# Kernel tuning notes

Hardware: AMD Instinct MI355X
Metric: run time of the kernel (lower is better)

The kernel has to match this reference:

```python
import jax, jax.numpy as jnp
import numpy as np

EMBED = 1024
HEADS = 16
HEAD_DIM = EMBED // HEADS


def setup_inputs() -> dict:
    key = jax.random.key(0)
    k1, k2, k3, k4, k5 = jax.random.split(key, 5)
    B, S = 4, 2048
    scale = 1.0 / np.sqrt(EMBED)
    return {
        "query_features": jax.random.normal(k1, (B, S, EMBED), dtype=jnp.float32),
        "W_qkv": jax.random.normal(k2, (EMBED, 3 * EMBED), dtype=jnp.float32) * scale,
        "b_qkv": jnp.zeros((3 * EMBED,), dtype=jnp.float32),
        "W_out": jax.random.normal(k3, (EMBED, EMBED), dtype=jnp.float32) * scale,
        "b_out": jnp.zeros((EMBED,), dtype=jnp.float32),
    }


def reference(query_features, W_qkv, b_qkv, W_out, b_out):
    B, S, E = query_features.shape
    qkv = jnp.einsum("bse,ef->bsf", query_features, W_qkv) + b_qkv  # [B,S,3E]
    q, k, v = jnp.split(qkv, 3, axis=-1)
    # split heads: [B,H,S,D]
    def heads(x):
        return x.reshape(B, S, HEADS, HEAD_DIM).transpose(0, 2, 1, 3)
    q, k, v = heads(q), heads(k), heads(v)
    scale = 1.0 / np.sqrt(HEAD_DIM)
    scores = jnp.einsum("bhqd,bhkd->bhqk", q, k) * scale
    attn = jax.nn.softmax(scores, axis=-1)
    out = jnp.einsum("bhqk,bhkd->bhqd", attn, v)  # [B,H,S,D]
    out = out.transpose(0, 2, 1, 3).reshape(B, S, E)
    return jnp.einsum("bse,ef->bsf", out, W_out) + b_out
```

## Files before the change

### kernel.cpp

```cpp
#include <hip/hip_runtime.h>
#include <hip/hip_bf16.h>
#include <stdint.h>
#include <stddef.h>

using short8  = __attribute__((ext_vector_type(8))) short;
using short4v = __attribute__((ext_vector_type(4))) short;
using int4v   = __attribute__((ext_vector_type(4))) int;
using f32x4   = __attribute__((ext_vector_type(4))) float;
typedef __hip_bfloat16 bf16_t;

__device__ __forceinline__ void glds16(const void* g, const void* l) {
  __builtin_amdgcn_global_load_lds(
      (const __attribute__((address_space(1))) void*)g,
      (__attribute__((address_space(3))) void*)l, 16, 0, 0);
}
__device__ __forceinline__ short bfbits(float x) {
  bf16_t h = __float2bfloat16(x);
  return __builtin_bit_cast(short, h);
}
__device__ __forceinline__ int pk2(float lo, float hi) {
  return __builtin_amdgcn_perm(__builtin_bit_cast(unsigned, hi),
                               __builtin_bit_cast(unsigned, lo), 0x07060302u);
}

__global__ __launch_bounds__(256)
void preprocess(const void* __restrict__ Wqkv, bf16_t* __restrict__ WqkvT,
                const void* __restrict__ Wout, bf16_t* __restrict__ WoutT,
                const void* __restrict__ Xv, bf16_t* __restrict__ Xb,
                int* __restrict__ flag) {
  __shared__ int sbad;
  __shared__ float tile[32][33];
  const int tid = threadIdx.x;
  const int bid = blockIdx.x;
  if (tid == 0) sbad = 0;
  __syncthreads();
  {
    int bad = 0;
    const unsigned short* wp = (const unsigned short*)Wqkv;
#pragma unroll
    for (int j = 0; j < 4; ++j) {
      float f = __uint_as_float((unsigned)wp[tid + j * 256] << 16);
      if (!(fabsf(f) <= 1e10f)) bad = 1;
    }
    if (bad) sbad = 1;
  }
  __syncthreads();
  const int isf = sbad;
  if (bid == 0 && tid == 0) *flag = isf;

  if (bid < 4096) {
    int bx = bid & 127;
    const int by = bid >> 7;
    const int tx = tid & 31, ty = tid >> 5;
    const void* Wv;
    bf16_t* Wt;
    int C;
    if (bx < 96) {
      Wv = Wqkv; Wt = WqkvT; C = 3072;
    } else {
      bx -= 96; Wv = Wout; Wt = WoutT; C = 1024;
    }
    const int n0 = bx * 32, k0 = by * 32;
#pragma unroll
    for (int j = 0; j < 4; ++j) {
      const int k = k0 + ty + j * 8;
      tile[ty + j * 8][tx] =
          isf ? ((const float*)Wv)[(size_t)k * C + n0 + tx]
              : __bfloat162float(((const bf16_t*)Wv)[(size_t)k * C + n0 + tx]);
    }
    __syncthreads();
#pragma unroll
    for (int j = 0; j < 4; ++j) {
      const int n = n0 + ty + j * 8;
      Wt[(size_t)n * 1024 + k0 + tx] = __float2bfloat16(tile[tx][ty + j * 8]);
    }
  } else {
    const int i = ((bid - 4096) * 256 + tid) * 4;
    if (isf) {
      const float4 v = *(const float4*)((const float*)Xv + i);
      Xb[i + 0] = __float2bfloat16(v.x);
      Xb[i + 1] = __float2bfloat16(v.y);
      Xb[i + 2] = __float2bfloat16(v.z);
      Xb[i + 3] = __float2bfloat16(v.w);
    } else {
      *(uint2*)(Xb + i) = *(const uint2*)((const bf16_t*)Xv + i);
    }
  }
}

template <int MODE>
__global__ __launch_bounds__(256)
void gemm_k(const bf16_t* __restrict__ A, const bf16_t* __restrict__ Bt,
            const void* __restrict__ biasv, void* __restrict__ Cv,
            bf16_t* __restrict__ Qo, bf16_t* __restrict__ Ko,
            bf16_t* __restrict__ Vo, int M, int N, int K,
            const int* __restrict__ flag) {
  constexpr float CSC = 0.18033688011112042f;
  __shared__ __align__(16) bf16_t lA[2][128 * 64];
  __shared__ __align__(16) bf16_t lB[2][128 * 64];

  const int isf32 = *flag;
  const int tid  = threadIdx.x;
  const int w    = tid >> 6;
  const int lane = tid & 63;
  const int lrow = lane & 15;
  const int quad = lane >> 4;
  const int m0 = blockIdx.x * 128;
  const int n0 = blockIdx.y * 128;
  const int wm = (w >> 1) * 64;
  const int wn = (w & 1) * 64;

  f32x4 acc[4][4];
  for (int i = 0; i < 4; ++i)
    for (int j = 0; j < 4; ++j)
      for (int r = 0; r < 4; ++r) acc[i][j][r] = 0.f;

  const char* Ab = (const char*)A;
  const char* Bb = (const char*)Bt;
  unsigned aoff[4], boff[4];
  int ldst[4];
#pragma unroll
  for (int i = 0; i < 4; ++i) {
    const int cbase = i * 256 + w * 64;
    const int c = cbase + lane;
    const int row = c >> 3;
    const int q = (c & 7) ^ (row & 7);
    aoff[i] = (unsigned)((m0 + row) * K + q * 8) * 2u;
    boff[i] = (unsigned)((n0 + row) * K + q * 8) * 2u;
    ldst[i] = cbase * 16;
  }

  auto stage = [&](int buf, int kt) {
    const unsigned kb = (unsigned)kt * 2u;
#pragma unroll
    for (int i = 0; i < 4; ++i) {
      glds16(Ab + aoff[i] + kb, (const char*)lA[buf] + ldst[i]);
      glds16(Bb + boff[i] + kb, (const char*)lB[buf] + ldst[i]);
    }
  };

  stage(0, 0);
  __syncthreads();

  int buf = 0;
  for (int kt = 0; kt < K; kt += 64) {
    if (kt + 64 < K) stage(buf ^ 1, kt + 64);
    const char* la = (const char*)lA[buf];
    const char* lb = (const char*)lB[buf];
#pragma unroll
    for (int ks = 0; ks < 2; ++ks) {
      short8 af[4], bfr[4];
#pragma unroll
      for (int mi = 0; mi < 4; ++mi) {
        const int row = wm + mi * 16 + lrow;
        const int slot = (ks * 4 + quad) ^ (row & 7);
        af[mi] = *(const short8*)(la + row * 128 + slot * 16);
      }
#pragma unroll
      for (int ni = 0; ni < 4; ++ni) {
        const int row = wn + ni * 16 + lrow;
        const int slot = (ks * 4 + quad) ^ (row & 7);
        bfr[ni] = *(const short8*)(lb + row * 128 + slot * 16);
      }
#pragma unroll
      for (int mi = 0; mi < 4; ++mi)
#pragma unroll
        for (int ni = 0; ni < 4; ++ni)
          acc[mi][ni] = __builtin_amdgcn_mfma_f32_16x16x32_bf16(
              af[mi], bfr[ni], acc[mi][ni], 0, 0, 0);
    }
    __syncthreads();
    buf ^= 1;
  }

  if (MODE == 1) {
    const int sec = n0 >> 10;
    const int b = m0 >> 11;
    const int s0 = (m0 & 2047) + wm + quad * 4;
#pragma unroll
    for (int mi = 0; mi < 4; ++mi) {
#pragma unroll
      for (int ni = 0; ni < 4; ++ni) {
        const int col = n0 + wn + ni * 16 + lrow;
        const float bv = isf32 ? ((const float*)biasv)[col]
                               : __bfloat162float(((const bf16_t*)biasv)[col]);
        const int h = (col >> 6) & 15, d = col & 63;
        const int s = s0 + mi * 16;
        if (sec == 2) {
          short4v hv4;
#pragma unroll
          for (int r = 0; r < 4; ++r) hv4[r] = bfbits(acc[mi][ni][r] + bv);
          *(short4v*)(Vo + ((((size_t)b * 16 + h) * 64) + d) * 2048 + s) = hv4;
        } else if (sec == 0) {
          bf16_t* dst = Qo + ((((size_t)b * 16 + h) * 2048) + s) * 64 + d;
#pragma unroll
          for (int r = 0; r < 4; ++r)
            dst[(size_t)r * 64] = __float2bfloat16((acc[mi][ni][r] + bv) * CSC);
        } else {
          bf16_t* dst = Ko + ((((size_t)b * 16 + h) * 2048) + s) * 64 + d;
#pragma unroll
          for (int r = 0; r < 4; ++r)
            dst[(size_t)r * 64] = __float2bfloat16(acc[mi][ni][r] + bv);
        }
      }
    }
  } else {
#pragma unroll
    for (int mi = 0; mi < 4; ++mi) {
#pragma unroll
      for (int ni = 0; ni < 4; ++ni) {
        const int col = n0 + wn + ni * 16 + lrow;
        const float bv = isf32 ? ((const float*)biasv)[col]
                               : __bfloat162float(((const bf16_t*)biasv)[col]);
#pragma unroll
        for (int r = 0; r < 4; ++r) {
          const int row = m0 + wm + mi * 16 + quad * 4 + r;
          const float val = acc[mi][ni][r] + bv;
          if (isf32)
            ((float*)Cv)[(size_t)row * N + col] = val;
          else
            ((bf16_t*)Cv)[(size_t)row * N + col] = __float2bfloat16(val);
        }
      }
    }
  }
}

__global__ __launch_bounds__(256, 2)
void attn_fwd(const bf16_t* __restrict__ Q, const bf16_t* __restrict__ K,
              const bf16_t* __restrict__ Vt, bf16_t* __restrict__ AO) {
  __shared__ __align__(16) bf16_t lK[2][64 * 64];
  __shared__ __align__(16) bf16_t lV[2][64 * 64];

  const int tid  = threadIdx.x;
  const int w    = tid >> 6;
  const int lane = tid & 63;
  const int lrow = lane & 15;
  const int quad = lane >> 4;
  const int id = blockIdx.x;
  const int swz = (id & 7) * 64 + (id >> 3);
  const int bh  = swz >> 3;
  const int q0  = (swz & 7) * 256;

  const bf16_t* Qb = Q + (size_t)bh * 2048 * 64;
  const bf16_t* Kb = K + (size_t)bh * 2048 * 64;
  const bf16_t* Vb = Vt + (size_t)bh * 64 * 2048;

  const int rbase = (lrow >> 2) * 8 + (lrow & 3);
  const int fkl   = 2 * (lrow >> 2) + (lrow & 1);

  short8 aq[4][2];
#pragma unroll
  for (int qt = 0; qt < 4; ++qt)
#pragma unroll
    for (int ks = 0; ks < 2; ++ks)
      aq[qt][ks] = *(const short8*)(Qb +
          (size_t)(q0 + w * 64 + qt * 16 + lrow) * 64 + ks * 32 + quad * 8);

  short8 ones;
#pragma unroll
  for (int j = 0; j < 8; ++j) ones[j] = (short)0x3F80;

  const f32x4 zf = {0.f, 0.f, 0.f, 0.f};

  f32x4 ot[4][4];
  f32x4 lsacc[4];
#pragma unroll
  for (int dt = 0; dt < 4; ++dt)
#pragma unroll
    for (int qt = 0; qt < 4; ++qt)
#pragma unroll
      for (int r = 0; r < 4; ++r) ot[dt][qt][r] = 0.f;
#pragma unroll
  for (int qt = 0; qt < 4; ++qt)
#pragma unroll
    for (int r = 0; r < 4; ++r) lsacc[qt][r] = 0.f;

  auto stage = [&](int buf, int kt) {
#pragma unroll
    for (int i = 0; i < 2; ++i) {
      const int cbase = i * 256 + w * 64;
      const int c = cbase + lane;
      const int row = c >> 3, ch = c & 7;
      const int fk = 2 * ((row >> 3) & 3) + (row & 1);
      glds16(Kb + (size_t)(kt + row) * 64 + (ch ^ fk) * 8,
             (const char*)lK[buf] + cbase * 16);
      glds16(Vb + (size_t)row * 2048 + kt + (ch ^ (row & 7)) * 8,
             (const char*)lV[buf] + cbase * 16);
    }
  };

  auto compute = [&](const bf16_t* lKb, const bf16_t* lVb) {
    f32x4 sc[2][2][4];
#pragma unroll
    for (int g = 0; g < 2; ++g) {
      short8 ak0[2], ak1[2];
#pragma unroll
      for (int T = 0; T < 2; ++T) {
        const int row = g * 32 + T * 4 + rbase;
        ak0[T] = *(const short8*)((const char*)lKb + row * 128 +
                                  ((0 * 4 + quad) ^ fkl) * 16);
        ak1[T] = *(const short8*)((const char*)lKb + row * 128 +
                                  ((1 * 4 + quad) ^ fkl) * 16);
      }
      __builtin_amdgcn_s_setprio(1);
#pragma unroll
      for (int T = 0; T < 2; ++T)
#pragma unroll
        for (int qt = 0; qt < 4; ++qt)
          sc[g][T][qt] = __builtin_amdgcn_mfma_f32_16x16x32_bf16(
              ak0[T], aq[qt][0], zf, 0, 0, 0);
#pragma unroll
      for (int T = 0; T < 2; ++T)
#pragma unroll
        for (int qt = 0; qt < 4; ++qt)
          sc[g][T][qt] = __builtin_amdgcn_mfma_f32_16x16x32_bf16(
              ak1[T], aq[qt][1], sc[g][T][qt], 0, 0, 0);
      __builtin_amdgcn_s_setprio(0);
    }
#pragma unroll
    for (int g = 0; g < 2; ++g) {
      short8 pb[4];
#pragma unroll
      for (int qt = 0; qt < 4; ++qt) {
        float p[8];
#pragma unroll
        for (int T = 0; T < 2; ++T)
#pragma unroll
          for (int r = 0; r < 4; ++r)
            p[T * 4 + r] = __builtin_amdgcn_exp2f(sc[g][T][qt][r]);
        int4v pi = {pk2(p[0], p[1]), pk2(p[2], p[3]), pk2(p[4], p[5]),
                    pk2(p[6], p[7])};
        pb[qt] = __builtin_bit_cast(short8, pi);
      }

      __builtin_amdgcn_s_setprio(1);
#pragma unroll
      for (int qt = 0; qt < 4; ++qt)
        lsacc[qt] = __builtin_amdgcn_mfma_f32_16x16x32_bf16(ones, pb[qt],
                                                            lsacc[qt], 0, 0, 0);
#pragma unroll
      for (int dt = 0; dt < 4; ++dt) {
        const int row = dt * 16 + lrow;
        const int slot = (g * 4 + quad) ^ (row & 7);
        const short8 vf =
            *(const short8*)((const char*)lVb + row * 128 + slot * 16);
#pragma unroll
        for (int qt = 0; qt < 4; ++qt)
          ot[dt][qt] = __builtin_amdgcn_mfma_f32_16x16x32_bf16(
              vf, pb[qt], ot[dt][qt], 0, 0, 0);
      }
      __builtin_amdgcn_s_setprio(0);
    }
  };

  stage(0, 0);
  __syncthreads();

  for (int kt = 0; kt < 2048; kt += 128) {
    if (kt + 64 < 2048) stage(1, kt + 64);
    compute(lK[0], lV[0]);
    __syncthreads();
    if (kt + 128 < 2048) stage(0, kt + 128);
    compute(lK[1], lV[1]);
    __syncthreads();
  }

  const int b = bh >> 4, h = bh & 15;
#pragma unroll
  for (int qt = 0; qt < 4; ++qt) {
    const float inv = 1.f / lsacc[qt][0];
    const int srow = q0 + w * 64 + qt * 16 + lrow;
#pragma unroll
    for (int dt = 0; dt < 4; ++dt) {
      uint2 pack;
      short* ps = (short*)&pack;
#pragma unroll
      for (int r = 0; r < 4; ++r) ps[r] = bfbits(ot[dt][qt][r] * inv);
      *(uint2*)(AO + ((size_t)b * 2048 + srow) * 1024 + h * 64 + dt * 16 +
                quad * 4) = pack;
    }
  }
}

extern "C" void kernel_launch(void* const* d_in, const int* in_sizes, int n_in,
                              void* d_out, int out_size, void* d_ws,
                              size_t ws_size, hipStream_t stream) {
  const void* X    = d_in[0];
  const void* Wqkv = d_in[1];
  const void* bqkv = d_in[2];
  const void* Wout = d_in[3];
  const void* bout = d_in[4];

  char* ws = (char*)d_ws;
  bf16_t* WqkvT = (bf16_t*)(ws);
  bf16_t* WoutT = (bf16_t*)(ws + 6291456);
  bf16_t* Qw    = (bf16_t*)(ws + 8388608);
  bf16_t* Kw    = (bf16_t*)(ws + 25165824);
  bf16_t* Vw    = (bf16_t*)(ws + 41943040);
  bf16_t* AOw   = (bf16_t*)(ws + 58720256);
  bf16_t* Xbf   = AOw;
  int*    flag  = (int*)(ws + 75497472);

  preprocess<<<12288, 256, 0, stream>>>(Wqkv, WqkvT, Wout, WoutT, X, Xbf, flag);

  gemm_k<1><<<dim3(64, 24), 256, 0, stream>>>(Xbf, WqkvT, bqkv, nullptr, Qw,
                                              Kw, Vw, 8192, 3072, 1024, flag);
  attn_fwd<<<512, 256, 0, stream>>>(Qw, Kw, Vw, AOw);
  gemm_k<0><<<dim3(64, 8), 256, 0, stream>>>(AOw, WoutT, bout, d_out, nullptr,
                                             nullptr, nullptr, 8192, 1024, 1024,
                                             flag);
}
```

Before: 258.1 us.

## Enlarge GEMM block tile to 256x128 with 512 threads, single-buffered LDS

The GEMM kernel now uses 8 waves per block covering a 256x128 output tile instead of 4 waves covering 128x128, so each B tile loaded into LDS is reused across more rows and the grid has half as many blocks. The LDS double buffer is dropped: each k-step loads into a single buffer, synchronizes, computes, then synchronizes again. This cuts LDS footprint and global reloads of B, but loads no longer overlap with MFMA work. The output-projection GEMM grid becomes only 256 blocks, which may underfill the device.

```diff
diff --git a/kernel.cpp b/kernel.cpp
--- a/kernel.cpp
+++ b/kernel.cpp
@@ -89,15 +89,15 @@
 }
 
 template <int MODE>
-__global__ __launch_bounds__(256)
+__global__ __launch_bounds__(512)
 void gemm_k(const bf16_t* __restrict__ A, const bf16_t* __restrict__ Bt,
             const void* __restrict__ biasv, void* __restrict__ Cv,
             bf16_t* __restrict__ Qo, bf16_t* __restrict__ Ko,
             bf16_t* __restrict__ Vo, int M, int N, int K,
             const int* __restrict__ flag) {
   constexpr float CSC = 0.18033688011112042f;
-  __shared__ __align__(16) bf16_t lA[2][128 * 64];
-  __shared__ __align__(16) bf16_t lB[2][128 * 64];
+  __shared__ __align__(16) bf16_t lA[256 * 64];
+  __shared__ __align__(16) bf16_t lB[128 * 64];
 
   const int isf32 = *flag;
   const int tid  = threadIdx.x;
@@ -105,7 +105,7 @@
   const int lane = tid & 63;
   const int lrow = lane & 15;
   const int quad = lane >> 4;
-  const int m0 = blockIdx.x * 128;
+  const int m0 = blockIdx.x * 256;
   const int n0 = blockIdx.y * 128;
   const int wm = (w >> 1) * 64;
   const int wn = (w & 1) * 64;
@@ -117,36 +117,38 @@
 
   const char* Ab = (const char*)A;
   const char* Bb = (const char*)Bt;
-  unsigned aoff[4], boff[4];
-  int ldst[4];
+  unsigned aoff[4], boff[2];
+  int lda[4], ldb[2];
 #pragma unroll
   for (int i = 0; i < 4; ++i) {
-    const int cbase = i * 256 + w * 64;
-    const int c = cbase + lane;
+    const int c = i * 512 + tid;
     const int row = c >> 3;
     const int q = (c & 7) ^ (row & 7);
     aoff[i] = (unsigned)((m0 + row) * K + q * 8) * 2u;
+    lda[i] = c * 16;
+  }
+#pragma unroll
+  for (int i = 0; i < 2; ++i) {
+    const int c = i * 512 + tid;
+    const int row = c >> 3;
+    const int q = (c & 7) ^ (row & 7);
     boff[i] = (unsigned)((n0 + row) * K + q * 8) * 2u;
-    ldst[i] = cbase * 16;
-  }
-
-  auto stage = [&](int buf, int kt) {
+    ldb[i] = c * 16;
+  }
+
+  auto stage = [&](int kt) {
     const unsigned kb = (unsigned)kt * 2u;
 #pragma unroll
-    for (int i = 0; i < 4; ++i) {
-      glds16(Ab + aoff[i] + kb, (const char*)lA[buf] + ldst[i]);
-      glds16(Bb + boff[i] + kb, (const char*)lB[buf] + ldst[i]);
-    }
+    for (int i = 0; i < 4; ++i)
+      glds16(Ab + aoff[i] + kb, (const char*)lA + lda[i]);
+#pragma unroll
+    for (int i = 0; i < 2; ++i)
+      glds16(Bb + boff[i] + kb, (const char*)lB + ldb[i]);
   };
 
-  stage(0, 0);
-  __syncthreads();
-
-  int buf = 0;
   for (int kt = 0; kt < K; kt += 64) {
-    if (kt + 64 < K) stage(buf ^ 1, kt + 64);
-    const char* la = (const char*)lA[buf];
-    const char* lb = (const char*)lB[buf];
+    stage(kt);
+    __syncthreads();
 #pragma unroll
     for (int ks = 0; ks < 2; ++ks) {
       short8 af[4], bfr[4];
@@ -154,13 +156,13 @@
       for (int mi = 0; mi < 4; ++mi) {
         const int row = wm + mi * 16 + lrow;
         const int slot = (ks * 4 + quad) ^ (row & 7);
-        af[mi] = *(const short8*)(la + row * 128 + slot * 16);
+        af[mi] = *(const short8*)((const char*)lA + row * 128 + slot * 16);
       }
 #pragma unroll
       for (int ni = 0; ni < 4; ++ni) {
         const int row = wn + ni * 16 + lrow;
         const int slot = (ks * 4 + quad) ^ (row & 7);
-        bfr[ni] = *(const short8*)(lb + row * 128 + slot * 16);
+        bfr[ni] = *(const short8*)((const char*)lB + row * 128 + slot * 16);
       }
 #pragma unroll
       for (int mi = 0; mi < 4; ++mi)
@@ -170,7 +172,6 @@
               af[mi], bfr[ni], acc[mi][ni], 0, 0, 0);
     }
     __syncthreads();
-    buf ^= 1;
   }
 
   if (MODE == 1) {
@@ -404,10 +405,10 @@
 
   preprocess<<<12288, 256, 0, stream>>>(Wqkv, WqkvT, Wout, WoutT, X, Xbf, flag);
 
-  gemm_k<1><<<dim3(64, 24), 256, 0, stream>>>(Xbf, WqkvT, bqkv, nullptr, Qw,
+  gemm_k<1><<<dim3(32, 24), 512, 0, stream>>>(Xbf, WqkvT, bqkv, nullptr, Qw,
                                               Kw, Vw, 8192, 3072, 1024, flag);
   attn_fwd<<<512, 256, 0, stream>>>(Qw, Kw, Vw, AOw);
-  gemm_k<0><<<dim3(64, 8), 256, 0, stream>>>(AOw, WoutT, bout, d_out, nullptr,
+  gemm_k<0><<<dim3(32, 8), 512, 0, stream>>>(AOw, WoutT, bout, d_out, nullptr,
                                              nullptr, nullptr, 8192, 1024, 1024,
                                              flag);
 }
```

New measurement: 249.8 us. 3.2% less time.
